# Performance work log

Hardware: AMD Instinct MI355X
Metric: run time of the kernel (lower is better)

## Reference

```python
import jax, jax.numpy as jnp
import numpy as np


def setup_inputs() -> dict:
    key = jax.random.key(0)
    k1, k2 = jax.random.split(key)
    x1 = jax.random.normal(k1, (2048, 64), dtype=jnp.float32)
    x2 = jax.random.normal(k2, (2048, 64), dtype=jnp.float32)
    return {"x1": x1, "x2": x2}


def reference(x1, x2):
    # Faithful to L1Distance._dist with postprocess=identity (gpytorch default),
    # x1_eq_x2=False.
    adjustment = jnp.mean(x1, axis=-2, keepdims=True)  # [1, D]
    x1c = x1 - adjustment
    x2c = x2 - adjustment
    # pairwise L1: [N1, N2, D] broadcast, abs, sum over D -> [N1, N2]
    res = jnp.sum(jnp.abs(x1c[:, None, :] - x2c[None, :, :]), axis=-1)
    res = jnp.maximum(res, 0.0)  # clamp_min_(0)
    return res
```

## Files before the change

### kernel.cpp

```cpp
#include <hip/hip_runtime.h>


#define D_FIXED 64
#define BI 128
#define BJ 64
#define PAD 68

__global__ __launch_bounds__(256, 2)
void l1dist_kernel(const float* __restrict__ x1, const float* __restrict__ x2,
                   float* __restrict__ out, int N1, int N2) {
    __shared__ float s1[BI * PAD];
    __shared__ float s2[BJ * PAD];

    const int tx = threadIdx.x;
    const int ty = threadIdx.y;
    const int t  = ty * 16 + tx;
    const int i0 = blockIdx.y * BI;
    const int j0 = blockIdx.x * BJ;

    const float* g1 = x1 + (size_t)i0 * D_FIXED;
    #pragma unroll
    for (int f = 0; f < 8; ++f) {
        int idx = t + f * 256;
        int row = idx >> 4;
        int c4  = (idx & 15) << 2;
        *(float4*)(s1 + row * PAD + c4) = *(const float4*)(g1 + row * D_FIXED + c4);
    }
    const float* g2 = x2 + (size_t)j0 * D_FIXED;
    #pragma unroll
    for (int f = 0; f < 4; ++f) {
        int idx = t + f * 256;
        int row = idx >> 4;
        int c4  = (idx & 15) << 2;
        *(float4*)(s2 + row * PAD + c4) = *(const float4*)(g2 + row * D_FIXED + c4);
    }
    __syncthreads();

    float acc[8][4];
    #pragma unroll
    for (int r = 0; r < 8; ++r)
        #pragma unroll
        for (int c = 0; c < 4; ++c) acc[r][c] = 0.0f;

    #pragma unroll
    for (int d = 0; d < D_FIXED; d += 4) {
        float4 a[8], b[4];
        #pragma unroll
        for (int c = 0; c < 4; ++c)
            b[c] = *(const float4*)(s2 + (tx + 16 * c) * PAD + d);
        #pragma unroll
        for (int r = 0; r < 8; ++r)
            a[r] = *(const float4*)(s1 + (ty + 16 * r) * PAD + d);

        #pragma unroll
        for (int r = 0; r < 8; ++r) {
            #pragma unroll
            for (int c = 0; c < 4; ++c) {
                float d0 = a[r].x - b[c].x;
                float d1 = a[r].y - b[c].y;
                float d2 = a[r].z - b[c].z;
                float d3 = a[r].w - b[c].w;
                acc[r][c] += (fabsf(d0) + fabsf(d1)) + (fabsf(d2) + fabsf(d3));
            }
        }
    }

    #pragma unroll
    for (int r = 0; r < 8; ++r) {
        const size_t i = i0 + ty + 16 * r;
        #pragma unroll
        for (int c = 0; c < 4; ++c) {
            const int j = j0 + tx + 16 * c;
            __builtin_nontemporal_store(acc[r][c], &out[i * N2 + j]);
        }
    }
}

extern "C" void kernel_launch(void* const* d_in, const int* in_sizes, int n_in,
                              void* d_out, int out_size, void* d_ws, size_t ws_size,
                              hipStream_t stream) {
    const float* x1 = (const float*)d_in[0];
    const float* x2 = (const float*)d_in[1];
    float* out = (float*)d_out;

    const int N1 = in_sizes[0] / D_FIXED;
    const int N2 = in_sizes[1] / D_FIXED;

    dim3 block(16, 16);
    dim3 grid(N2 / BJ, N1 / BI);
    l1dist_kernel<<<grid, block, 0, stream>>>(x1, x2, out, N1, N2);
}
```

Before: 69.89 us.

## Replace LDS-tiled L1 distance with register-resident x2 rows and broadcast x1 loads

```diff
diff --git a/kernel.cpp b/kernel.cpp
--- a/kernel.cpp
+++ b/kernel.cpp
@@ -2,77 +2,42 @@
 
 
 #define D_FIXED 64
-#define BI 128
-#define BJ 64
-#define PAD 68
+#define ROWS 32
+#define JT   64
 
-__global__ __launch_bounds__(256, 2)
+__global__ __launch_bounds__(64, 2)
 void l1dist_kernel(const float* __restrict__ x1, const float* __restrict__ x2,
                    float* __restrict__ out, int N1, int N2) {
-    __shared__ float s1[BI * PAD];
-    __shared__ float s2[BJ * PAD];
+    const int lane = threadIdx.x;
+    const int j0 = blockIdx.x * JT;
+    const int i0 = blockIdx.y * ROWS;
 
-    const int tx = threadIdx.x;
-    const int ty = threadIdx.y;
-    const int t  = ty * 16 + tx;
-    const int i0 = blockIdx.y * BI;
-    const int j0 = blockIdx.x * BJ;
+    const float4* xb = (const float4*)(x2 + (size_t)(j0 + lane) * D_FIXED);
+    float4 b[16];
+    #pragma unroll
+    for (int q = 0; q < 16; ++q) b[q] = xb[q];
 
-    const float* g1 = x1 + (size_t)i0 * D_FIXED;
-    #pragma unroll
-    for (int f = 0; f < 8; ++f) {
-        int idx = t + f * 256;
-        int row = idx >> 4;
-        int c4  = (idx & 15) << 2;
-        *(float4*)(s1 + row * PAD + c4) = *(const float4*)(g1 + row * D_FIXED + c4);
-    }
-    const float* g2 = x2 + (size_t)j0 * D_FIXED;
-    #pragma unroll
-    for (int f = 0; f < 4; ++f) {
-        int idx = t + f * 256;
-        int row = idx >> 4;
-        int c4  = (idx & 15) << 2;
-        *(float4*)(s2 + row * PAD + c4) = *(const float4*)(g2 + row * D_FIXED + c4);
-    }
-    __syncthreads();
+    const float* a = x1 + (size_t)i0 * D_FIXED;
+    float* o = out + (size_t)i0 * N2 + (j0 + lane);
 
-    float acc[8][4];
-    #pragma unroll
-    for (int r = 0; r < 8; ++r)
+    #pragma unroll 2
+    for (int r = 0; r < ROWS; ++r) {
+        float p0 = 0.f, p1 = 0.f, p2 = 0.f, p3 = 0.f;
         #pragma unroll
-        for (int c = 0; c < 4; ++c) acc[r][c] = 0.0f;
-
-    #pragma unroll
-    for (int d = 0; d < D_FIXED; d += 4) {
-        float4 a[8], b[4];
-        #pragma unroll
-        for (int c = 0; c < 4; ++c)
-            b[c] = *(const float4*)(s2 + (tx + 16 * c) * PAD + d);
-        #pragma unroll
-        for (int r = 0; r < 8; ++r)
-            a[r] = *(const float4*)(s1 + (ty + 16 * r) * PAD + d);
-
-        #pragma unroll
-        for (int r = 0; r < 8; ++r) {
-            #pragma unroll
-            for (int c = 0; c < 4; ++c) {
-                float d0 = a[r].x - b[c].x;
-                float d1 = a[r].y - b[c].y;
-                float d2 = a[r].z - b[c].z;
-                float d3 = a[r].w - b[c].w;
-                acc[r][c] += (fabsf(d0) + fabsf(d1)) + (fabsf(d2) + fabsf(d3));
-            }
+        for (int q = 0; q < 16; ++q) {
+            const float4 bb = b[q];
+            const float a0 = a[4 * q + 0];
+            const float a1 = a[4 * q + 1];
+            const float a2 = a[4 * q + 2];
+            const float a3 = a[4 * q + 3];
+            p0 += fabsf(a0 - bb.x);
+            p1 += fabsf(a1 - bb.y);
+            p2 += fabsf(a2 - bb.z);
+            p3 += fabsf(a3 - bb.w);
         }
-    }
-
-    #pragma unroll
-    for (int r = 0; r < 8; ++r) {
-        const size_t i = i0 + ty + 16 * r;
-        #pragma unroll
-        for (int c = 0; c < 4; ++c) {
-            const int j = j0 + tx + 16 * c;
-            __builtin_nontemporal_store(acc[r][c], &out[i * N2 + j]);
-        }
+        __builtin_nontemporal_store((p0 + p1) + (p2 + p3), o);
+        a += D_FIXED;
+        o += N2;
     }
 }
 
@@ -83,10 +48,10 @@
     const float* x2 = (const float*)d_in[1];
     float* out = (float*)d_out;
 
-    const int N1 = in_sizes[0] / D_FIXED;
-    const int N2 = in_sizes[1] / D_FIXED;
+    const int n1 = in_sizes[0] / D_FIXED;
+    const int n2 = in_sizes[1] / D_FIXED;
 
-    dim3 block(16, 16);
-    dim3 grid(N2 / BJ, N1 / BI);
-    l1dist_kernel<<<grid, block, 0, stream>>>(x1, x2, out, N1, N2);
+    dim3 block(JT);
+    dim3 grid(n2 / JT, n1 / ROWS);
+    l1dist_kernel<<<grid, block, 0, stream>>>(x1, x2, out, n1, n2);
 }
```

New measurement: 89.45 us. 28.0% more time.

## Double-buffer LDS tile loads and use packed float2 subtraction

Applied to the files above, without the earlier changes.

```diff
diff --git a/kernel.cpp b/kernel.cpp
--- a/kernel.cpp
+++ b/kernel.cpp
@@ -5,6 +5,36 @@
 #define BI 128
 #define BJ 64
 #define PAD 68
+
+typedef float v2f __attribute__((ext_vector_type(2)));
+
+#define LOAD_TILE(A_, B_, dd)                                              \
+    {                                                                      \
+        _Pragma("unroll")                                                  \
+        for (int c = 0; c < 4; ++c)         \
+            B_[c] = *(const float4*)(s2 + (tx + 16 * c) * PAD + (dd));     \
+        _Pragma("unroll")                                                  \
+        for (int r = 0; r < 8; ++r)     \
+            A_[r] = *(const float4*)(s1 + (ty + 16 * r) * PAD + (dd));     \
+    }
+
+#define COMP_TILE(A_, B_)                                                  \
+    {                                                                      \
+        _Pragma("unroll")                                                  \
+        for (int r = 0; r < 8; ++r) {                                      \
+            const v2f alo = {A_[r].x, A_[r].y};                            \
+            const v2f ahi = {A_[r].z, A_[r].w};                            \
+            _Pragma("unroll")                                              \
+            for (int c = 0; c < 4; ++c) {                                  \
+                const v2f blo = {B_[c].x, B_[c].y};                        \
+                const v2f bhi = {B_[c].z, B_[c].w};                        \
+                const v2f dlo = alo - blo;     \
+                const v2f dhi = ahi - bhi;                                 \
+                acc[r][c] += (fabsf(dlo.x) + fabsf(dlo.y)) +               \
+                             (fabsf(dhi.x) + fabsf(dhi.y));                \
+            }                                                              \
+        }                                                                  \
+    }
 
 __global__ __launch_bounds__(256, 2)
 void l1dist_kernel(const float* __restrict__ x1, const float* __restrict__ x2,
@@ -42,27 +72,16 @@
         #pragma unroll
         for (int c = 0; c < 4; ++c) acc[r][c] = 0.0f;
 
+    float4 Ae[8], Be[4], Ao[8], Bo[4];
+    LOAD_TILE(Ae, Be, 0);
+
     #pragma unroll
-    for (int d = 0; d < D_FIXED; d += 4) {
-        float4 a[8], b[4];
-        #pragma unroll
-        for (int c = 0; c < 4; ++c)
-            b[c] = *(const float4*)(s2 + (tx + 16 * c) * PAD + d);
-        #pragma unroll
-        for (int r = 0; r < 8; ++r)
-            a[r] = *(const float4*)(s1 + (ty + 16 * r) * PAD + d);
-
-        #pragma unroll
-        for (int r = 0; r < 8; ++r) {
-            #pragma unroll
-            for (int c = 0; c < 4; ++c) {
-                float d0 = a[r].x - b[c].x;
-                float d1 = a[r].y - b[c].y;
-                float d2 = a[r].z - b[c].z;
-                float d3 = a[r].w - b[c].w;
-                acc[r][c] += (fabsf(d0) + fabsf(d1)) + (fabsf(d2) + fabsf(d3));
-            }
-        }
+    for (int s = 0; s < 16; s += 2) {
+        LOAD_TILE(Ao, Bo, (s + 1) * 4);
+        COMP_TILE(Ae, Be);
+        if (s + 2 < 16)
+            LOAD_TILE(Ae, Be, (s + 2) * 4);
+        COMP_TILE(Ao, Bo);
     }
 
     #pragma unroll
```

Result: slower. 276.6 us (+295.8%).
